# Optimization experiments

Measured on AMD Instinct MI355X. Metric: run time of the kernel, lower is better.

## Reference

```python
import jax, jax.numpy as jnp
import numpy as np

D_MODEL = 1024
NUM_HEADS = 16
D_K = D_MODEL // NUM_HEADS


def setup_inputs() -> dict:
    key = jax.random.key(0)
    ks = jax.random.split(key, 12)
    B, S = 2, 2048
    s = 1.0 / np.sqrt(D_MODEL)
    inp = {
        "query": jax.random.normal(ks[0], (B, S, D_MODEL), jnp.float32),
        "key": jax.random.normal(ks[1], (B, S, D_MODEL), jnp.float32),
        "value": jax.random.normal(ks[2], (B, S, D_MODEL), jnp.float32),
        "w_q": jax.random.normal(ks[3], (D_MODEL, D_MODEL), jnp.float32) * s,
        "b_q": jax.random.normal(ks[4], (D_MODEL,), jnp.float32) * 0.01,
        "w_k": jax.random.normal(ks[5], (D_MODEL, D_MODEL), jnp.float32) * s,
        "b_k": jax.random.normal(ks[6], (D_MODEL,), jnp.float32) * 0.01,
        "w_v": jax.random.normal(ks[7], (D_MODEL, D_MODEL), jnp.float32) * s,
        "b_v": jax.random.normal(ks[8], (D_MODEL,), jnp.float32) * 0.01,
        "w_o": jax.random.normal(ks[9], (D_MODEL, D_MODEL), jnp.float32) * s,
        "b_o": jax.random.normal(ks[10], (D_MODEL,), jnp.float32) * 0.01,
    }
    return inp


def _split_heads(x):
    # [B, S, d_model] -> [B, H, S, d_k]
    B, S, _ = x.shape
    return x.reshape(B, S, NUM_HEADS, D_K).transpose(0, 2, 1, 3)


def reference(query, key, value, w_q, b_q, w_k, b_k, w_v, b_v, w_o, b_o):
    B, S, _ = query.shape
    Q = _split_heads(query @ w_q.T + b_q)
    K = _split_heads(key @ w_k.T + b_k)
    V = _split_heads(value @ w_v.T + b_v)
    scale = 1.0 / jnp.sqrt(jnp.asarray(D_K, Q.dtype))
    scores = jnp.einsum("bhqd,bhkd->bhqk", Q, K) * scale  # [B,H,S,S]
    attn = jax.nn.softmax(scores, axis=-1)
    ctx = jnp.einsum("bhqk,bhkd->bhqd", attn, V)
    ctx = ctx.transpose(0, 2, 1, 3).reshape(B, S, D_MODEL)
    return ctx @ w_o.T + b_o
```

## Files before the change

kernel.cpp:

```cpp
#include <hip/hip_runtime.h>
#include <hip/hip_bf16.h>
#include <stdint.h>

#define D_MODEL 1024
#define NHEAD   16
#define DK      64
#define SEQ     2048
#define BATCH   2

using bf16 = __bf16;
typedef __bf16 bf16x8 __attribute__((ext_vector_type(8)));
typedef float  f32x4  __attribute__((ext_vector_type(4)));
typedef float  f32x16 __attribute__((ext_vector_type(16)));
typedef unsigned uintx2 __attribute__((ext_vector_type(2)));

__device__ __forceinline__ unsigned short f2bf(float x) {
  return __builtin_bit_cast(unsigned short, (__bf16)x);
}
__device__ __forceinline__ unsigned pk2bf(float a, float b) {
  return (unsigned)f2bf(a) | ((unsigned)f2bf(b) << 16);
}
__device__ __forceinline__ float uasf(unsigned x) {
  return __builtin_bit_cast(float, x);
}
__device__ __forceinline__ unsigned fasu(float x) {
  return __builtin_bit_cast(unsigned, x);
}

__device__ __forceinline__ void gld_lds16(const void* g, void* l) {
  __builtin_amdgcn_global_load_lds(
      (const __attribute__((address_space(1))) void*)g,
      (__attribute__((address_space(3))) void*)l, 16, 0, 0);
}

__device__ __forceinline__ float xhalf_sum(float x) {
  uintx2 r = __builtin_amdgcn_permlane32_swap(fasu(x), fasu(x), false, false);
  return uasf(r[0]) + uasf(r[1]);
}

#define MHA_PACK(sv, off, dst)                                           \
  {                                                                      \
    float e0 = __builtin_amdgcn_exp2f(sv[off + 0]);                      \
    float e1 = __builtin_amdgcn_exp2f(sv[off + 1]);                      \
    float e2 = __builtin_amdgcn_exp2f(sv[off + 2]);                      \
    float e3 = __builtin_amdgcn_exp2f(sv[off + 3]);                      \
    float e4 = __builtin_amdgcn_exp2f(sv[off + 4]);                      \
    float e5 = __builtin_amdgcn_exp2f(sv[off + 5]);                      \
    float e6 = __builtin_amdgcn_exp2f(sv[off + 6]);                      \
    float e7 = __builtin_amdgcn_exp2f(sv[off + 7]);                      \
    ps += ((e0 + e1) + (e2 + e3)) + ((e4 + e5) + (e6 + e7));             \
    unsigned c0 = pk2bf(e0, e1), c1 = pk2bf(e2, e3);                     \
    unsigned c2 = pk2bf(e4, e5), c3 = pk2bf(e6, e7);                     \
    uintx2 r02 = __builtin_amdgcn_permlane32_swap(c0, c2, false, false); \
    uintx2 r13 = __builtin_amdgcn_permlane32_swap(c1, c3, false, false); \
    uint4 w; w.x = r02[0]; w.y = r13[0]; w.z = r02[1]; w.w = r13[1];     \
    dst = __builtin_bit_cast(bf16x8, w);                                 \
  }

struct ConvArgs {
  const float* src[7];
  bf16* dst[7];
};

__global__ __launch_bounds__(256) void convert_f32_bf16(ConvArgs a) {
  int v = blockIdx.x * 256 + threadIdx.x;
  int seg, off;
  if (v < 3 * 1048576) { seg = v >> 20; off = v & (1048576 - 1); }
  else { int u = v - 3 * 1048576; seg = 3 + (u >> 18); off = u & (262144 - 1); }
  float4 f = ((const float4*)a.src[seg])[off];
  ushort4 o;
  o.x = f2bf(f.x); o.y = f2bf(f.y); o.z = f2bf(f.z); o.w = f2bf(f.w);
  ((ushort4*)a.dst[seg])[off] = o;
}

template <int BM>
__device__ __forceinline__ void gemm_core(
    const bf16* __restrict__ A, const bf16* __restrict__ B,
    const float* __restrict__ bias, void* __restrict__ Cout,
    int mode, int bx, int by, float oscale, char* lds) {
  bf16* As = (bf16*)lds;
  bf16* Bs = (bf16*)(lds + BM * 128);
  constexpr int FM = BM / 32;
  const int tid  = threadIdx.x;
  const int lane = tid & 63;
  const int wave = tid >> 6;
  const int wr = wave >> 1, wc = wave & 1;
  const int t = lane >> 4, q = lane & 15;

  f32x4 acc[FM][4];
#pragma unroll
  for (int i = 0; i < FM; ++i)
#pragma unroll
    for (int j = 0; j < 4; ++j) acc[i][j] = (f32x4){0.f, 0.f, 0.f, 0.f};

  const char* Abase = (const char*)(A + (size_t)bx * BM * D_MODEL);
  const char* Bbase = (const char*)(B + (size_t)by * 128 * D_MODEL);

  for (int kt = 0; kt < D_MODEL / 64; ++kt) {
#pragma unroll
    for (int i = 0; i < BM / 32; ++i) {
      int c = tid + i * 256;
      int row = c >> 3, cb = c & 7;
      int src = (cb * 16) ^ ((row & 7) << 4);
      gld_lds16(Abase + (size_t)row * (D_MODEL * 2) + kt * 128 + src,
                (char*)As + c * 16);
    }
#pragma unroll
    for (int i = 0; i < 4; ++i) {
      int c = tid + i * 256;
      int row = c >> 3, cb = c & 7;
      int src = (cb * 16) ^ ((row & 7) << 4);
      gld_lds16(Bbase + (size_t)row * (D_MODEL * 2) + kt * 128 + src,
                (char*)Bs + c * 16);
    }
    asm volatile("s_waitcnt vmcnt(0)" ::: "memory");
    __syncthreads();
#pragma unroll
    for (int ks = 0; ks < 2; ++ks) {
      bf16x8 af[FM], bfv[4];
#pragma unroll
      for (int f = 0; f < FM; ++f) {
        int ra = wr * (BM / 2) + f * 16 + q;
        af[f] = *(const bf16x8*)((const char*)As + ra * 128 +
                                 ((ks * 64 + t * 16) ^ ((ra & 7) << 4)));
      }
#pragma unroll
      for (int f = 0; f < 4; ++f) {
        int rb = wc * 64 + f * 16 + q;
        bfv[f] = *(const bf16x8*)((const char*)Bs + rb * 128 +
                                  ((ks * 64 + t * 16) ^ ((rb & 7) << 4)));
      }
#pragma unroll
      for (int fm = 0; fm < FM; ++fm)
#pragma unroll
        for (int fn = 0; fn < 4; ++fn)
          acc[fm][fn] = __builtin_amdgcn_mfma_f32_16x16x32_bf16(
              af[fm], bfv[fn], acc[fm][fn], 0, 0, 0);
    }
    __syncthreads();
  }

#pragma unroll
  for (int fm = 0; fm < FM; ++fm)
#pragma unroll
    for (int fn = 0; fn < 4; ++fn)
#pragma unroll
      for (int jj = 0; jj < 4; ++jj) {
        int m = bx * BM + wr * (BM / 2) + fm * 16 + t * 4 + jj;
        int n = by * 128 + wc * 64 + fn * 16 + q;
        float v = acc[fm][fn][jj];
        if (mode == 0) {
          v = (v + bias[n]) * oscale;
          int b = m >> 11, s = m & (SEQ - 1), h = n >> 6, d = n & 63;
          ((bf16*)Cout)[(((size_t)(b * NHEAD + h)) * SEQ + s) * DK + d] = (bf16)v;
        } else if (mode == 1) {
          v += bias[m];
          int h = m >> 6, d = m & 63, b = n >> 11, s = n & (SEQ - 1);
          ((bf16*)Cout)[(((size_t)(b * NHEAD + h)) * DK + d) * SEQ + s] = (bf16)v;
        } else {
          v += bias[n];
          ((float*)Cout)[(size_t)m * D_MODEL + n] = v;
        }
      }
}

struct QkvArgs {
  const bf16* A[3]; const bf16* B[3]; const float* bias[3]; bf16* out[3];
};

__global__ __launch_bounds__(256) void gemm_qkv(QkvArgs a) {
  __shared__ char lds[128 * 128 + 128 * 128];
  int z = blockIdx.z;
  int mode = (z == 2) ? 1 : 0;
  int bx = (z == 2) ? blockIdx.y : blockIdx.x;
  int by = (z == 2) ? blockIdx.x : blockIdx.y;
  float osc = (z == 0) ? 0.18033688011112042f : 1.0f;
  gemm_core<128>(a.A[z], a.B[z], a.bias[z], a.out[z], mode, bx, by, osc, lds);
}

__global__ __launch_bounds__(256) void gemm_o(
    const bf16* __restrict__ A, const bf16* __restrict__ B,
    const float* __restrict__ bias, float* __restrict__ Cout) {
  __shared__ char lds[64 * 128 + 128 * 128];
  gemm_core<64>(A, B, bias, Cout, 2, blockIdx.x, blockIdx.y, 1.0f, lds);
}

__global__ __launch_bounds__(512, 2) void flash_attn(
    const bf16* __restrict__ Qh, const bf16* __restrict__ Kh,
    const bf16* __restrict__ Vt, bf16* __restrict__ ctx) {
  __shared__ char lds[65536];
  const int tid  = threadIdx.x;
  const int lane = tid & 63;
  const int wave = tid >> 6;
  const int lo = lane & 31;
  const int hi = lane >> 5;
  const int grp = wave >> 2;
  const int wq  = wave & 3;
  const int bh = blockIdx.x;
  const int q0 = blockIdx.y * 128 + wq * 32;

  const bf16* Qb = Qh + (size_t)bh * SEQ * DK;
  const char* Kb = (const char*)(Kh + (size_t)bh * SEQ * DK) + grp * 1024 * 128;
  const char* Vb = (const char*)(Vt + (size_t)bh * DK * SEQ) + grp * 1024 * 2;
  char* Kg = lds + grp * 16384;
  char* Vg = lds + 32768 + grp * 16384;

  bf16x8 qf[4];
#pragma unroll
  for (int c = 0; c < 4; ++c)
    qf[c] = *(const bf16x8*)(Qb + (size_t)(q0 + lo) * DK + c * 16 + hi * 8);

  const int tg = tid & 255;
  const int srow = tg >> 3;
  const int ssrc = ((tg & 7) * 16) ^ ((srow & 7) << 4);
  const char* gK0 = Kb + (size_t)srow * 128 + ssrc;
  const char* gK1 = Kb + (size_t)(srow + 32) * 128 + ssrc;
  const char* gV0 = Vb + (size_t)srow * 4096 + ssrc;
  const char* gV1 = Vb + (size_t)(srow + 32) * 4096 + ssrc;
  char* sK0 = Kg + tg * 16;
  char* sK1 = Kg + 4096 + tg * 16;
  char* sV0 = Vg + tg * 16;
  char* sV1 = Vg + 4096 + tg * 16;

  const int key = (lo & 7) << 4;
  const char* KA[4]; const char* VA[4];
#pragma unroll
  for (int c = 0; c < 4; ++c) {
    int o = (((2 * c + hi) * 16) ^ key) + lo * 128;
    KA[c] = Kg + o;
    VA[c] = Vg + o;
  }

  f32x16 acc0 = {}, acc1 = {};
  float lsum = 0.f;

  gld_lds16(gK0, sK0); gld_lds16(gK1, sK1);
  gld_lds16(gV0, sV0); gld_lds16(gV1, sV1);
  __syncthreads();

  auto tile = [&](int kt, int CUR) {
    if (kt + 1 < 16) {
      int nb = CUR ^ 8192;
      gld_lds16(gK0 + (kt + 1) * 8192, sK0 + nb);
      gld_lds16(gK1 + (kt + 1) * 8192, sK1 + nb);
      gld_lds16(gV0 + (kt + 1) * 128,  sV0 + nb);
      gld_lds16(gV1 + (kt + 1) * 128,  sV1 + nb);
    }

    float ps = 0.f;
    bf16x8 pa[4];

    {
      bf16x8 kf[4];
#pragma unroll
      for (int c = 0; c < 4; ++c) kf[c] = *(const bf16x8*)(KA[c] + CUR);
      f32x16 s0 = {};
      __builtin_amdgcn_s_setprio(1);
#pragma unroll
      for (int c = 0; c < 4; ++c)
        s0 = __builtin_amdgcn_mfma_f32_32x32x16_bf16(kf[c], qf[c], s0, 0, 0, 0);
      __builtin_amdgcn_s_setprio(0);
      MHA_PACK(s0, 0, pa[0]);
      MHA_PACK(s0, 8, pa[1]);
    }

    {
      bf16x8 kf[4];
#pragma unroll
      for (int c = 0; c < 4; ++c) kf[c] = *(const bf16x8*)(KA[c] + CUR + 4096);
      f32x16 s1 = {};
      __builtin_amdgcn_s_setprio(1);
#pragma unroll
      for (int c = 0; c < 4; ++c)
        s1 = __builtin_amdgcn_mfma_f32_32x32x16_bf16(kf[c], qf[c], s1, 0, 0, 0);
      __builtin_amdgcn_s_setprio(0);
      MHA_PACK(s1, 0, pa[2]);
      MHA_PACK(s1, 8, pa[3]);
    }
    lsum += ps;

    bf16x8 vf[2][4];
#pragma unroll
    for (int ks = 0; ks < 4; ++ks) {
      vf[0][ks] = *(const bf16x8*)(VA[ks] + CUR);
      vf[1][ks] = *(const bf16x8*)(VA[ks] + CUR + 4096);
    }
    __builtin_amdgcn_s_setprio(1);
#pragma unroll
    for (int ks = 0; ks < 4; ++ks) {
      acc0 = __builtin_amdgcn_mfma_f32_32x32x16_bf16(pa[ks], vf[0][ks], acc0, 0, 0, 0);
      acc1 = __builtin_amdgcn_mfma_f32_32x32x16_bf16(pa[ks], vf[1][ks], acc1, 0, 0, 0);
    }
    __builtin_amdgcn_s_setprio(0);

    __syncthreads();
  };

  for (int kt = 0; kt < 16; kt += 2) {
    tile(kt, 0);
    tile(kt + 1, 8192);
  }

  float lrun = xhalf_sum(lsum);

  float* lsh = (float*)lds;
  float* U1  = (float*)(lds + 4096);
  if (hi == 0) lsh[grp * 128 + wq * 32 + lo] = lrun;
  if (grp == 1) {
    float* dst = U1 + (size_t)(wq * 64 + lane) * 33;
#pragma unroll
    for (int r = 0; r < 16; ++r) { dst[r] = acc0[r]; dst[16 + r] = acc1[r]; }
  }
  __syncthreads();
  if (grp == 0) {
    const float* src = U1 + (size_t)(wq * 64 + lane) * 33;
    int b = bh >> 4, h = bh & 15;
#pragma unroll
    for (int r = 0; r < 16; ++r) {
      int row = (r & 3) + 8 * (r >> 2) + 4 * hi;
      int gr = wq * 32 + row;
      float linv = 1.f / (lsh[gr] + lsh[128 + gr]);
      float o0 = (acc0[r] + src[r]) * linv;
      float o1 = (acc1[r] + src[16 + r]) * linv;
      int srw = q0 + row;
      size_t base = ((size_t)(b * SEQ + srw)) * D_MODEL + h * 64 + lo;
      ctx[base]      = (bf16)o0;
      ctx[base + 32] = (bf16)o1;
    }
  }
}

extern "C" void kernel_launch(void* const* d_in, const int* in_sizes, int n_in,
                              void* d_out, int out_size, void* d_ws, size_t ws_size,
                              hipStream_t stream) {
  const float* query = (const float*)d_in[0];
  const float* key_  = (const float*)d_in[1];
  const float* value = (const float*)d_in[2];
  const float* w_q = (const float*)d_in[3];
  const float* b_q = (const float*)d_in[4];
  const float* w_k = (const float*)d_in[5];
  const float* b_k = (const float*)d_in[6];
  const float* w_v = (const float*)d_in[7];
  const float* b_v = (const float*)d_in[8];
  const float* w_o = (const float*)d_in[9];
  const float* b_o = (const float*)d_in[10];

  char* ws = (char*)d_ws;
  const size_t MB = 1024 * 1024;
  bf16* bQ  = (bf16*)(ws + 0 * MB);
  bf16* bK  = (bf16*)(ws + 8 * MB);
  bf16* bV  = (bf16*)(ws + 16 * MB);
  bf16* bWq = (bf16*)(ws + 24 * MB);
  bf16* bWk = (bf16*)(ws + 26 * MB);
  bf16* bWv = (bf16*)(ws + 28 * MB);
  bf16* bWo = (bf16*)(ws + 30 * MB);
  bf16* Qh  = (bf16*)(ws + 32 * MB);
  bf16* Kh  = (bf16*)(ws + 40 * MB);
  bf16* Vth = (bf16*)(ws + 48 * MB);
  bf16* ctx = (bf16*)(ws + 56 * MB);

  ConvArgs ca;
  ca.src[0] = query; ca.src[1] = key_; ca.src[2] = value;
  ca.src[3] = w_q;   ca.src[4] = w_k;  ca.src[5] = w_v; ca.src[6] = w_o;
  ca.dst[0] = bQ;  ca.dst[1] = bK;  ca.dst[2] = bV;
  ca.dst[3] = bWq; ca.dst[4] = bWk; ca.dst[5] = bWv; ca.dst[6] = bWo;
  convert_f32_bf16<<<16384, 256, 0, stream>>>(ca);

  QkvArgs qa;
  qa.A[0] = bQ;  qa.B[0] = bWq; qa.bias[0] = b_q; qa.out[0] = Qh;
  qa.A[1] = bK;  qa.B[1] = bWk; qa.bias[1] = b_k; qa.out[1] = Kh;
  qa.A[2] = bWv; qa.B[2] = bV;  qa.bias[2] = b_v; qa.out[2] = Vth;
  gemm_qkv<<<dim3(32, 8, 3), 256, 0, stream>>>(qa);

  flash_attn<<<dim3(32, 16), 512, 0, stream>>>(Qh, Kh, Vth, ctx);

  gemm_o<<<dim3(64, 8), 256, 0, stream>>>(ctx, bWo, b_o, (float*)d_out);
}
```

Measured before the change: 142.8 us.

## Double-buffer LDS tiles in GEMM core to overlap loads with MFMA

```diff
diff --git a/kernel.cpp b/kernel.cpp
--- a/kernel.cpp
+++ b/kernel.cpp
@@ -78,9 +78,9 @@
     const bf16* __restrict__ A, const bf16* __restrict__ B,
     const float* __restrict__ bias, void* __restrict__ Cout,
     int mode, int bx, int by, float oscale, char* lds) {
-  bf16* As = (bf16*)lds;
-  bf16* Bs = (bf16*)(lds + BM * 128);
-  constexpr int FM = BM / 32;
+  constexpr int FM   = BM / 32;
+  constexpr int ACH  = BM / 32;
+  constexpr int HALF = BM * 128 + 16384;
   const int tid  = threadIdx.x;
   const int lane = tid & 63;
   const int wave = tid >> 6;
@@ -96,48 +96,74 @@
   const char* Abase = (const char*)(A + (size_t)bx * BM * D_MODEL);
   const char* Bbase = (const char*)(B + (size_t)by * 128 * D_MODEL);
 
-  for (int kt = 0; kt < D_MODEL / 64; ++kt) {
-#pragma unroll
-    for (int i = 0; i < BM / 32; ++i) {
-      int c = tid + i * 256;
-      int row = c >> 3, cb = c & 7;
-      int src = (cb * 16) ^ ((row & 7) << 4);
-      gld_lds16(Abase + (size_t)row * (D_MODEL * 2) + kt * 128 + src,
-                (char*)As + c * 16);
-    }
-#pragma unroll
-    for (int i = 0; i < 4; ++i) {
-      int c = tid + i * 256;
-      int row = c >> 3, cb = c & 7;
-      int src = (cb * 16) ^ ((row & 7) << 4);
-      gld_lds16(Bbase + (size_t)row * (D_MODEL * 2) + kt * 128 + src,
-                (char*)Bs + c * 16);
-    }
-    asm volatile("s_waitcnt vmcnt(0)" ::: "memory");
-    __syncthreads();
+  const char* gA[ACH]; char* sA[ACH];
+  const char* gB[4];   char* sB[4];
+#pragma unroll
+  for (int i = 0; i < ACH; ++i) {
+    int c = tid + i * 256, row = c >> 3;
+    int src = ((c & 7) * 16) ^ ((row & 7) << 4);
+    gA[i] = Abase + (size_t)row * (D_MODEL * 2) + src;
+    sA[i] = lds + c * 16;
+  }
+#pragma unroll
+  for (int i = 0; i < 4; ++i) {
+    int c = tid + i * 256, row = c >> 3;
+    int src = ((c & 7) * 16) ^ ((row & 7) << 4);
+    gB[i] = Bbase + (size_t)row * (D_MODEL * 2) + src;
+    sB[i] = lds + BM * 128 + c * 16;
+  }
+
+  const char* aA[FM][2]; const char* aB[4][2];
+#pragma unroll
+  for (int f = 0; f < FM; ++f)
+#pragma unroll
+    for (int ks = 0; ks < 2; ++ks) {
+      int ra = wr * (BM / 2) + f * 16 + q;
+      aA[f][ks] = lds + ra * 128 + ((ks * 64 + t * 16) ^ ((q & 7) << 4));
+    }
+#pragma unroll
+  for (int f = 0; f < 4; ++f)
+#pragma unroll
+    for (int ks = 0; ks < 2; ++ks) {
+      int rb = wc * 64 + f * 16 + q;
+      aB[f][ks] = lds + BM * 128 + rb * 128 + ((ks * 64 + t * 16) ^ ((q & 7) << 4));
+    }
+
+#pragma unroll
+  for (int i = 0; i < ACH; ++i) gld_lds16(gA[i], sA[i]);
+#pragma unroll
+  for (int i = 0; i < 4; ++i)  gld_lds16(gB[i], sB[i]);
+  __syncthreads();
+
+  auto ktile = [&](int kt, int CUR) {
+    if (kt + 1 < D_MODEL / 64) {
+      int NXT = CUR ^ HALF;
+#pragma unroll
+      for (int i = 0; i < ACH; ++i) gld_lds16(gA[i] + (kt + 1) * 128, sA[i] + NXT);
+#pragma unroll
+      for (int i = 0; i < 4; ++i)  gld_lds16(gB[i] + (kt + 1) * 128, sB[i] + NXT);
+    }
 #pragma unroll
     for (int ks = 0; ks < 2; ++ks) {
       bf16x8 af[FM], bfv[4];
 #pragma unroll
-      for (int f = 0; f < FM; ++f) {
-        int ra = wr * (BM / 2) + f * 16 + q;
-        af[f] = *(const bf16x8*)((const char*)As + ra * 128 +
-                                 ((ks * 64 + t * 16) ^ ((ra & 7) << 4)));
-      }
-#pragma unroll
-      for (int f = 0; f < 4; ++f) {
-        int rb = wc * 64 + f * 16 + q;
-        bfv[f] = *(const bf16x8*)((const char*)Bs + rb * 128 +
-                                  ((ks * 64 + t * 16) ^ ((rb & 7) << 4)));
-      }
+      for (int f = 0; f < FM; ++f) af[f] = *(const bf16x8*)(aA[f][ks] + CUR);
+#pragma unroll
+      for (int f = 0; f < 4; ++f)  bfv[f] = *(const bf16x8*)(aB[f][ks] + CUR);
+      __builtin_amdgcn_s_setprio(1);
 #pragma unroll
       for (int fm = 0; fm < FM; ++fm)
 #pragma unroll
         for (int fn = 0; fn < 4; ++fn)
           acc[fm][fn] = __builtin_amdgcn_mfma_f32_16x16x32_bf16(
               af[fm], bfv[fn], acc[fm][fn], 0, 0, 0);
+      __builtin_amdgcn_s_setprio(0);
     }
     __syncthreads();
+  };
+  for (int kt = 0; kt < D_MODEL / 64; kt += 2) {
+    ktile(kt, 0);
+    ktile(kt + 1, HALF);
   }
 
 #pragma unroll
@@ -168,8 +194,8 @@
   const bf16* A[3]; const bf16* B[3]; const float* bias[3]; bf16* out[3];
 };
 
-__global__ __launch_bounds__(256) void gemm_qkv(QkvArgs a) {
-  __shared__ char lds[128 * 128 + 128 * 128];
+__global__ __launch_bounds__(256, 2) void gemm_qkv(QkvArgs a) {
+  __shared__ char lds[2 * (128 * 128 + 16384)];
   int z = blockIdx.z;
   int mode = (z == 2) ? 1 : 0;
   int bx = (z == 2) ? blockIdx.y : blockIdx.x;
@@ -178,10 +204,10 @@
   gemm_core<128>(a.A[z], a.B[z], a.bias[z], a.out[z], mode, bx, by, osc, lds);
 }
 
-__global__ __launch_bounds__(256) void gemm_o(
+__global__ __launch_bounds__(256, 2) void gemm_o(
     const bf16* __restrict__ A, const bf16* __restrict__ B,
     const float* __restrict__ bias, float* __restrict__ Cout) {
-  __shared__ char lds[64 * 128 + 128 * 128];
+  __shared__ char lds[2 * (64 * 128 + 16384)];
   gemm_core<64>(A, B, bias, Cout, 2, blockIdx.x, blockIdx.y, 1.0f, lds);
 }
 
```

After: 136.3 us, median of 2. -4.6%, faster.
